# Optimization experiments

Measured on AMD Instinct MI355X. Metric: run time of the kernel, lower is better.

The kernel has to match this reference:

```python
import jax, jax.numpy as jnp
import numpy as np

B, D, L, H = 2, 64, 512, 1024  # batch, n_docs (timesteps), tokens per doc, bert hidden


def _ln(x, g, b):
    # torch.nn.LayerNorm over last dim, eps=1e-5
    m = jnp.mean(x, axis=-1, keepdims=True)
    v = jnp.mean((x - m) ** 2, axis=-1, keepdims=True)
    return (x - m) / jnp.sqrt(v + 1e-5) * g + b


def _ht(x):
    # Hardtanh(min=-8, max=8)
    return jnp.clip(x, -8.0, 8.0)


def setup_inputs() -> dict:
    key = jax.random.key(0)
    ks = jax.random.split(key, 12)
    xavier = lambda k, shape: jax.random.normal(k, shape, dtype=jnp.float32) * np.float32(np.sqrt(2.0 / sum(shape)))
    return {
        "trans": jax.random.normal(ks[0], (B, D, L, H), dtype=jnp.float32) * 0.1,  # frozen BERT last_hidden_state
        "document_mask": jax.random.bernoulli(ks[1], 0.9, (B, D)),
        "Wf": xavier(ks[2], (H, H)), "bf": jnp.ones((H,), jnp.float32),
        "Wi": xavier(ks[3], (H, H)), "bi": jnp.zeros((H,), jnp.float32),
        "Wg": xavier(ks[4], (H, H)), "bg": jnp.zeros((H,), jnp.float32),
        "Wo": xavier(ks[5], (H, H)), "bo": jnp.zeros((H,), jnp.float32),
        "Wp": xavier(ks[6], (H, H)), "bp": jnp.zeros((H,), jnp.float32),
        "tF": xavier(ks[7], (L,)), "tI": xavier(ks[8], (L,)), "tO": xavier(ks[9], (L,)),
        "c_gamma": jnp.ones((H,), jnp.float32), "c_beta": jnp.zeros((H,), jnp.float32),
        "h_gamma": jnp.ones((H,), jnp.float32), "h_beta": jnp.zeros((H,), jnp.float32),
    }


def _forward(trans, document_mask, Wf, bf, Wi, bi, Wg, bg, Wo, bo, Wp, bp,
             tF, tI, tO, c_gamma, c_beta, h_gamma, h_beta):
    b, d, l, h = trans.shape
    # docFlat @ transform: contract the token (l) axis -> [b, d, h]
    pF = jnp.einsum('bdlh,l->bdh', trans, tF)
    pI = jnp.einsum('bdlh,l->bdh', trans, tI)
    pO = jnp.einsum('bdlh,l->bdh', trans, tO)

    def step(carry, xs):
        c, hs = carry                      # each [b, h]
        pf, pi, po, m = xs                 # [b, h] x3, [b] bool
        nC = _ln(c, c_gamma, c_beta)
        nH = _ln(hs, h_gamma, h_beta)
        f = jax.nn.sigmoid(_ht(nH @ Wf.T + bf) + pf)
        c2 = c * f
        i = jax.nn.sigmoid(_ht(nH @ Wi.T + bi) + pi)
        g = _ht(jax.nn.gelu(nH @ Wg.T + bg, approximate=False) + pi)
        c2 = c2 + i * g
        o = jax.nn.sigmoid(_ht(nH @ Wo.T + bo) + po)
        h2 = o * _ht(jax.nn.gelu(nC @ Wp.T + bp, approximate=False))
        mm = m[:, None]
        h2 = jnp.where(mm, h2, hs)
        c2 = jnp.where(mm, c2, c)
        c2 = jnp.clip(c2, -10.0, 10.0)
        h2 = jnp.clip(h2, -10.0, 10.0)
        return (c2, h2), None

    init = (jnp.zeros((b, h), trans.dtype), jnp.zeros((b, h), trans.dtype))
    xs = (pF.transpose(1, 0, 2), pI.transpose(1, 0, 2), pO.transpose(1, 0, 2), document_mask.T)
    (c_fin, h_fin), _ = jax.lax.scan(step, init, xs)
    return h_fin  # [b, h] (original returns [b, h, 1])


def reference(trans, document_mask, Wf, bf, Wi, bi, Wg, bg, Wo, bo, Wp, bp,
              tF, tI, tO, c_gamma, c_beta, h_gamma, h_beta):
    return _forward(trans, document_mask, Wf, bf, Wi, bi, Wg, bg, Wo, bo, Wp, bp,
                    tF, tI, tO, c_gamma, c_beta, h_gamma, h_beta)
```

## Files before the change

### kernel.cpp

```cpp
#include <hip/hip_runtime.h>
#include <math.h>


#define NBLK 256

__device__ __forceinline__ float sigf(float x)   { return 1.0f / (1.0f + __expf(-x)); }
__device__ __forceinline__ float geluf(float x)  { return 0.5f * x * (1.0f + erff(x * 0.70710678118654752f)); }
__device__ __forceinline__ float clampf(float x, float lo, float hi) { return fminf(fmaxf(x, lo), hi); }

__device__ __forceinline__ void astf(float* p, float v) {
    __hip_atomic_store(p, v, __ATOMIC_RELAXED, __HIP_MEMORY_SCOPE_AGENT);
}
__device__ __forceinline__ float aldf(const float* p) {
    return __hip_atomic_load(p, __ATOMIC_RELAXED, __HIP_MEMORY_SCOPE_AGENT);
}
__device__ __forceinline__ void astu(unsigned* p, unsigned v) {
    __hip_atomic_store(p, v, __ATOMIC_RELAXED, __HIP_MEMORY_SCOPE_AGENT);
}
__device__ __forceinline__ unsigned aldu(const unsigned* p) {
    return __hip_atomic_load(p, __ATOMIC_RELAXED, __HIP_MEMORY_SCOPE_AGENT);
}

__device__ __forceinline__ void gridbar(unsigned tgt, unsigned* flags, unsigned* rel,
                                        int blk, int t) {
    __syncthreads();
    if (t == 0) astu(&flags[blk], tgt);
    if (blk == 0) {
        if (t < 64) {
            for (;;) {
                unsigned a = aldu(&flags[t]);
                unsigned b = aldu(&flags[t + 64]);
                unsigned c = aldu(&flags[t + 128]);
                unsigned d = aldu(&flags[t + 192]);
                int ok = (a >= tgt) && (b >= tgt) && (c >= tgt) && (d >= tgt);
                if (__all(ok)) break;
                __builtin_amdgcn_s_sleep(1);
            }
            if (t == 0) astu(rel, tgt);
        }
    } else if (t == 0) {
        while (aldu(rel) < tgt) __builtin_amdgcn_s_sleep(2);
    }
    __syncthreads();
}

__global__ __launch_bounds__(256, 1) void fused_kernel(
    const float* __restrict__ trans, const int* __restrict__ mask,
    const float* __restrict__ Wf, const float* __restrict__ bf,
    const float* __restrict__ Wi, const float* __restrict__ bi,
    const float* __restrict__ Wg, const float* __restrict__ bg,
    const float* __restrict__ Wo, const float* __restrict__ bo,
    const float* __restrict__ Wp, const float* __restrict__ bp,
    const float* __restrict__ tF, const float* __restrict__ tI, const float* __restrict__ tO,
    const float* __restrict__ c_gamma, const float* __restrict__ c_beta,
    const float* __restrict__ h_gamma, const float* __restrict__ h_beta,
    float* __restrict__ ws, float* __restrict__ out)
{
    const int t    = threadIdx.x;
    const int lane = t & 63;
    const int wv   = t >> 6;
    const int blk  = blockIdx.x;
    const int hrow = (blk << 2) + wv;

    unsigned* flags = (unsigned*)ws;
    unsigned* rel   = flags + 256;
    float* stC = ws + 320;
    float* stH = ws + 4416;
    float* pF  = ws + 8512;
    float* pI  = pF + 131072;
    float* pO  = pI + 131072;

    __shared__ float smem[4][1024];
    __shared__ float red[4][8];

    float4 wfr[4], wir[4], wgr[4], wor[4], wpr[4];
    {
        const float4* rf = (const float4*)(Wf + (size_t)hrow * 1024);
        const float4* ri = (const float4*)(Wi + (size_t)hrow * 1024);
        const float4* rg = (const float4*)(Wg + (size_t)hrow * 1024);
        const float4* ro = (const float4*)(Wo + (size_t)hrow * 1024);
        const float4* rp = (const float4*)(Wp + (size_t)hrow * 1024);
        #pragma unroll
        for (int q = 0; q < 4; ++q) {
            const int k4 = lane + 64 * q;
            wfr[q] = rf[k4]; wir[q] = ri[k4]; wgr[q] = rg[k4];
            wor[q] = ro[k4]; wpr[q] = rp[k4];
        }
    }
    const float bfv = bf[hrow], biv = bi[hrow], bgv = bg[hrow], bov = bo[hrow], bpv = bp[hrow];

    {
        float* sF = &smem[0][0];
        float* sI = &smem[0][512];
        float* sO = &smem[1][0];
        sF[t] = tF[t]; sF[t + 256] = tF[t + 256];
        sI[t] = tI[t]; sI[t + 256] = tI[t + 256];
        sO[t] = tO[t]; sO[t + 256] = tO[t + 256];
        __syncthreads();

        const int bd = blk >> 1;
        const int h0 = (blk & 1) * 512;
        const int s  = t & 127;
        const int g  = t >> 7;
        const float4* tr = (const float4*)trans + (size_t)bd * 512 * 256 + (h0 >> 2) + s;

        float4 aF = make_float4(0.f,0.f,0.f,0.f);
        float4 aI = make_float4(0.f,0.f,0.f,0.f);
        float4 aO = make_float4(0.f,0.f,0.f,0.f);
        #pragma unroll 8
        for (int li = 0; li < 256; ++li) {
            const int l = g + 2 * li;
            float4 v = tr[(size_t)l * 256];
            const float wf = sF[l], wi = sI[l], wo = sO[l];
            aF.x = fmaf(v.x, wf, aF.x); aF.y = fmaf(v.y, wf, aF.y);
            aF.z = fmaf(v.z, wf, aF.z); aF.w = fmaf(v.w, wf, aF.w);
            aI.x = fmaf(v.x, wi, aI.x); aI.y = fmaf(v.y, wi, aI.y);
            aI.z = fmaf(v.z, wi, aI.z); aI.w = fmaf(v.w, wi, aI.w);
            aO.x = fmaf(v.x, wo, aO.x); aO.y = fmaf(v.y, wo, aO.y);
            aO.z = fmaf(v.z, wo, aO.z); aO.w = fmaf(v.w, wo, aO.w);
        }
        float4* cmb = (float4*)&smem[2][0];
        if (g == 1) { cmb[s] = aF; cmb[128 + s] = aI; cmb[256 + s] = aO; }
        __syncthreads();
        if (g == 0) {
            const float4 bF = cmb[s], bI = cmb[128 + s], bO = cmb[256 + s];
            aF.x += bF.x; aF.y += bF.y; aF.z += bF.z; aF.w += bF.w;
            aI.x += bI.x; aI.y += bI.y; aI.z += bI.z; aI.w += bI.w;
            aO.x += bO.x; aO.y += bO.y; aO.z += bO.z; aO.w += bO.w;
            const int base = bd * 1024 + h0 + 4 * s;
            astf(&pF[base+0], aF.x); astf(&pF[base+1], aF.y);
            astf(&pF[base+2], aF.z); astf(&pF[base+3], aF.w);
            astf(&pI[base+0], aI.x); astf(&pI[base+1], aI.y);
            astf(&pI[base+2], aI.z); astf(&pI[base+3], aI.w);
            astf(&pO[base+0], aO.x); astf(&pO[base+1], aO.y);
            astf(&pO[base+2], aO.z); astf(&pO[base+3], aO.w);
        }
    }
    gridbar(1u, flags, rel, blk, t);

    float cgv[4], cbv[4], hgv[4], hbv[4];
    #pragma unroll
    for (int j = 0; j < 4; ++j) {
        const int e = t + 256 * j;
        cgv[j] = c_gamma[e]; cbv[j] = c_beta[e];
        hgv[j] = h_gamma[e]; hbv[j] = h_beta[e];
    }

    for (int d = 0; d < 64; ++d) {
        const int par = d & 1;
        const float* cc = stC + par * 2048;
        const float* hc = stH + par * 2048;
        float* cn = stC + (par ^ 1) * 2048;
        float* hn = stH + (par ^ 1) * 2048;

        float pfv = 0.f, piv = 0.f, pov = 0.f;
        if (lane < 2) {
            const int pidx = (lane * 64 + d) * 1024 + hrow;
            pfv = aldf(&pF[pidx]); piv = aldf(&pI[pidx]); pov = aldf(&pO[pidx]);
        }

        float cv0[4], cv1[4], hv0[4], hv1[4];
        float s0=0,s1=0,s2=0,s3=0,s4=0,s5=0,s6=0,s7=0;
        #pragma unroll
        for (int j = 0; j < 4; ++j) {
            const int e = t + 256 * j;
            cv0[j] = aldf(cc + e);        cv1[j] = aldf(cc + 1024 + e);
            hv0[j] = aldf(hc + e);        hv1[j] = aldf(hc + 1024 + e);
        }
        #pragma unroll
        for (int j = 0; j < 4; ++j) {
            s0 += cv0[j]; s1 += cv0[j]*cv0[j];
            s2 += cv1[j]; s3 += cv1[j]*cv1[j];
            s4 += hv0[j]; s5 += hv0[j]*hv0[j];
            s6 += hv1[j]; s7 += hv1[j]*hv1[j];
        }
        #pragma unroll
        for (int off = 32; off; off >>= 1) {
            s0 += __shfl_xor(s0, off); s1 += __shfl_xor(s1, off);
            s2 += __shfl_xor(s2, off); s3 += __shfl_xor(s3, off);
            s4 += __shfl_xor(s4, off); s5 += __shfl_xor(s5, off);
            s6 += __shfl_xor(s6, off); s7 += __shfl_xor(s7, off);
        }
        if (lane == 0) {
            red[wv][0]=s0; red[wv][1]=s1; red[wv][2]=s2; red[wv][3]=s3;
            red[wv][4]=s4; red[wv][5]=s5; red[wv][6]=s6; red[wv][7]=s7;
        }
        __syncthreads();
        const float tc0 = red[0][0]+red[1][0]+red[2][0]+red[3][0];
        const float qc0 = red[0][1]+red[1][1]+red[2][1]+red[3][1];
        const float tc1 = red[0][2]+red[1][2]+red[2][2]+red[3][2];
        const float qc1 = red[0][3]+red[1][3]+red[2][3]+red[3][3];
        const float th0 = red[0][4]+red[1][4]+red[2][4]+red[3][4];
        const float qh0 = red[0][5]+red[1][5]+red[2][5]+red[3][5];
        const float th1 = red[0][6]+red[1][6]+red[2][6]+red[3][6];
        const float qh1 = red[0][7]+red[1][7]+red[2][7]+red[3][7];
        const float inv = 1.0f / 1024.0f;
        const float mc0 = tc0*inv, rc0 = rsqrtf(qc0*inv - mc0*mc0 + 1e-5f);
        const float mc1 = tc1*inv, rc1 = rsqrtf(qc1*inv - mc1*mc1 + 1e-5f);
        const float mh0 = th0*inv, rh0 = rsqrtf(qh0*inv - mh0*mh0 + 1e-5f);
        const float mh1 = th1*inv, rh1 = rsqrtf(qh1*inv - mh1*mh1 + 1e-5f);

        #pragma unroll
        for (int j = 0; j < 4; ++j) {
            const int e = t + 256 * j;
            smem[0][e] = (hv0[j]-mh0)*rh0*hgv[j] + hbv[j];
            smem[1][e] = (hv1[j]-mh1)*rh1*hgv[j] + hbv[j];
            smem[2][e] = (cv0[j]-mc0)*rc0*cgv[j] + cbv[j];
            smem[3][e] = (cv1[j]-mc1)*rc1*cgv[j] + cbv[j];
        }
        __syncthreads();

        float zf0=0,zf1=0,zi0=0,zi1=0,zg0=0,zg1=0,zo0=0,zo1=0,zp0=0,zp1=0;
        #pragma unroll
        for (int q = 0; q < 4; ++q) {
            const int k4 = lane + 64 * q;
            const float4 n0 = ((const float4*)smem[0])[k4];
            const float4 n1 = ((const float4*)smem[1])[k4];
            const float4 m0 = ((const float4*)smem[2])[k4];
            const float4 m1 = ((const float4*)smem[3])[k4];
            zf0 += wfr[q].x*n0.x + wfr[q].y*n0.y + wfr[q].z*n0.z + wfr[q].w*n0.w;
            zf1 += wfr[q].x*n1.x + wfr[q].y*n1.y + wfr[q].z*n1.z + wfr[q].w*n1.w;
            zi0 += wir[q].x*n0.x + wir[q].y*n0.y + wir[q].z*n0.z + wir[q].w*n0.w;
            zi1 += wir[q].x*n1.x + wir[q].y*n1.y + wir[q].z*n1.z + wir[q].w*n1.w;
            zg0 += wgr[q].x*n0.x + wgr[q].y*n0.y + wgr[q].z*n0.z + wgr[q].w*n0.w;
            zg1 += wgr[q].x*n1.x + wgr[q].y*n1.y + wgr[q].z*n1.z + wgr[q].w*n1.w;
            zo0 += wor[q].x*n0.x + wor[q].y*n0.y + wor[q].z*n0.z + wor[q].w*n0.w;
            zo1 += wor[q].x*n1.x + wor[q].y*n1.y + wor[q].z*n1.z + wor[q].w*n1.w;
            zp0 += wpr[q].x*m0.x + wpr[q].y*m0.y + wpr[q].z*m0.z + wpr[q].w*m0.w;
            zp1 += wpr[q].x*m1.x + wpr[q].y*m1.y + wpr[q].z*m1.z + wpr[q].w*m1.w;
        }
        #pragma unroll
        for (int off = 32; off; off >>= 1) {
            zf0 += __shfl_xor(zf0, off); zf1 += __shfl_xor(zf1, off);
            zi0 += __shfl_xor(zi0, off); zi1 += __shfl_xor(zi1, off);
            zg0 += __shfl_xor(zg0, off); zg1 += __shfl_xor(zg1, off);
            zo0 += __shfl_xor(zo0, off); zo1 += __shfl_xor(zo1, off);
            zp0 += __shfl_xor(zp0, off); zp1 += __shfl_xor(zp1, off);
        }

        if (lane < 2) {
            const int b = lane;
            const float zf = b ? zf1 : zf0;
            const float zi = b ? zi1 : zi0;
            const float zg = b ? zg1 : zg0;
            const float zo = b ? zo1 : zo0;
            const float zp = b ? zp1 : zp0;
            const float f  = sigf(clampf(zf + bfv, -8.f, 8.f) + pfv);
            const float ig = sigf(clampf(zi + biv, -8.f, 8.f) + piv);
            const float g  = clampf(geluf(zg + bgv) + piv, -8.f, 8.f);
            const float o  = sigf(clampf(zo + bov, -8.f, 8.f) + pov);
            const float hp = clampf(geluf(zp + bpv), -8.f, 8.f);
            const float co = aldf(cc + b * 1024 + hrow);
            const float ho = aldf(hc + b * 1024 + hrow);
            float c2 = co * f + ig * g;
            float h2 = o * hp;
            if (mask[b * 64 + d] == 0) { c2 = co; h2 = ho; }
            c2 = clampf(c2, -10.f, 10.f);
            h2 = clampf(h2, -10.f, 10.f);
            if (d == 63) {
                out[b * 1024 + hrow] = h2;
            } else {
                astf(cn + b * 1024 + hrow, c2);
                astf(hn + b * 1024 + hrow, h2);
            }
        }

        if (d == 63) break;
        gridbar((unsigned)(d + 2), flags, rel, blk, t);
    }
}

extern "C" void kernel_launch(void* const* d_in, const int* in_sizes, int n_in,
                              void* d_out, int out_size, void* d_ws, size_t ws_size,
                              hipStream_t stream)
{
    const float* trans = (const float*)d_in[0];
    const int*   mask  = (const int*)d_in[1];
    const float* Wf = (const float*)d_in[2];  const float* bf = (const float*)d_in[3];
    const float* Wi = (const float*)d_in[4];  const float* bi = (const float*)d_in[5];
    const float* Wg = (const float*)d_in[6];  const float* bg = (const float*)d_in[7];
    const float* Wo = (const float*)d_in[8];  const float* bo = (const float*)d_in[9];
    const float* Wp = (const float*)d_in[10]; const float* bp = (const float*)d_in[11];
    const float* tF = (const float*)d_in[12];
    const float* tI = (const float*)d_in[13];
    const float* tO = (const float*)d_in[14];
    const float* c_gamma = (const float*)d_in[15];
    const float* c_beta  = (const float*)d_in[16];
    const float* h_gamma = (const float*)d_in[17];
    const float* h_beta  = (const float*)d_in[18];

    float* ws  = (float*)d_ws;
    float* out = (float*)d_out;

    hipMemsetAsync(d_ws, 0, 8512u * sizeof(float), stream);

    void* args[] = { (void*)&trans, (void*)&mask,
                     (void*)&Wf, (void*)&bf, (void*)&Wi, (void*)&bi,
                     (void*)&Wg, (void*)&bg, (void*)&Wo, (void*)&bo,
                     (void*)&Wp, (void*)&bp,
                     (void*)&tF, (void*)&tI, (void*)&tO,
                     (void*)&c_gamma, (void*)&c_beta, (void*)&h_gamma, (void*)&h_beta,
                     (void*)&ws, (void*)&out };
    hipLaunchCooperativeKernel((void*)fused_kernel, dim3(256), dim3(256), args, 0, stream);
}
```

Before: 830.7 us.

## Replace per-step grid barrier with tagged 64-bit state values and polling

```diff
diff --git a/kernel.cpp b/kernel.cpp
--- a/kernel.cpp
+++ b/kernel.cpp
@@ -3,6 +3,7 @@
 
 
 #define NBLK 256
+typedef unsigned long long u64;
 
 __device__ __forceinline__ float sigf(float x)   { return 1.0f / (1.0f + __expf(-x)); }
 __device__ __forceinline__ float geluf(float x)  { return 0.5f * x * (1.0f + erff(x * 0.70710678118654752f)); }
@@ -18,6 +19,12 @@
     __hip_atomic_store(p, v, __ATOMIC_RELAXED, __HIP_MEMORY_SCOPE_AGENT);
 }
 __device__ __forceinline__ unsigned aldu(const unsigned* p) {
+    return __hip_atomic_load(p, __ATOMIC_RELAXED, __HIP_MEMORY_SCOPE_AGENT);
+}
+__device__ __forceinline__ void ast64(u64* p, u64 v) {
+    __hip_atomic_store(p, v, __ATOMIC_RELAXED, __HIP_MEMORY_SCOPE_AGENT);
+}
+__device__ __forceinline__ u64 ald64(const u64* p) {
     return __hip_atomic_load(p, __ATOMIC_RELAXED, __HIP_MEMORY_SCOPE_AGENT);
 }
 
@@ -64,14 +71,14 @@
 
     unsigned* flags = (unsigned*)ws;
     unsigned* rel   = flags + 256;
-    float* stC = ws + 320;
-    float* stH = ws + 4416;
-    float* pF  = ws + 8512;
+    u64* stC2 = (u64*)(ws + 320);
+    u64* stH2 = (u64*)(ws + 8512);
+    float* pF  = ws + 16704;
     float* pI  = pF + 131072;
     float* pO  = pI + 131072;
 
-    __shared__ float smem[4][1024];
-    __shared__ float red[4][8];
+    __shared__ float smem[2][4][1024];
+    __shared__ float red[2][4][8];
 
     float4 wfr[4], wir[4], wgr[4], wor[4], wpr[4];
     {
@@ -90,9 +97,9 @@
     const float bfv = bf[hrow], biv = bi[hrow], bgv = bg[hrow], bov = bo[hrow], bpv = bp[hrow];
 
     {
-        float* sF = &smem[0][0];
-        float* sI = &smem[0][512];
-        float* sO = &smem[1][0];
+        float* sF = &smem[0][0][0];
+        float* sI = &smem[0][0][512];
+        float* sO = &smem[0][1][0];
         sF[t] = tF[t]; sF[t + 256] = tF[t + 256];
         sI[t] = tI[t]; sI[t + 256] = tI[t + 256];
         sO[t] = tO[t]; sO[t + 256] = tO[t + 256];
@@ -119,7 +126,7 @@
             aO.x = fmaf(v.x, wo, aO.x); aO.y = fmaf(v.y, wo, aO.y);
             aO.z = fmaf(v.z, wo, aO.z); aO.w = fmaf(v.w, wo, aO.w);
         }
-        float4* cmb = (float4*)&smem[2][0];
+        float4* cmb = (float4*)&smem[0][2][0];
         if (g == 1) { cmb[s] = aF; cmb[128 + s] = aI; cmb[256 + s] = aO; }
         __syncthreads();
         if (g == 0) {
@@ -148,10 +155,12 @@
 
     for (int d = 0; d < 64; ++d) {
         const int par = d & 1;
-        const float* cc = stC + par * 2048;
-        const float* hc = stH + par * 2048;
-        float* cn = stC + (par ^ 1) * 2048;
-        float* hn = stH + (par ^ 1) * 2048;
+        const u64* cc2 = stC2 + par * 2048;
+        const u64* hc2 = stH2 + par * 2048;
+        u64* cn2 = stC2 + (par ^ 1) * 2048;
+        u64* hn2 = stH2 + (par ^ 1) * 2048;
+        float (*sm)[1024] = smem[par];
+        float (*rd)[8]    = red[par];
 
         float pfv = 0.f, piv = 0.f, pov = 0.f;
         if (lane < 2) {
@@ -159,16 +168,39 @@
             pfv = aldf(&pF[pidx]); piv = aldf(&pI[pidx]); pov = aldf(&pO[pidx]);
         }
 
+        u64 vc0[4], vc1[4], vh0[4], vh1[4];
+        u64 vco = 0, vho = 0;
+        const unsigned dtag = (unsigned)d;
+        for (;;) {
+            #pragma unroll
+            for (int j = 0; j < 4; ++j) {
+                const int e = t + 256 * j;
+                vc0[j] = ald64(cc2 + e);        vc1[j] = ald64(cc2 + 1024 + e);
+                vh0[j] = ald64(hc2 + e);        vh1[j] = ald64(hc2 + 1024 + e);
+            }
+            bool ok = true;
+            #pragma unroll
+            for (int j = 0; j < 4; ++j) {
+                ok = ok && ((unsigned)(vc0[j] >> 32) == dtag) && ((unsigned)(vc1[j] >> 32) == dtag)
+                        && ((unsigned)(vh0[j] >> 32) == dtag) && ((unsigned)(vh1[j] >> 32) == dtag);
+            }
+            if (lane < 2) {
+                vco = ald64(cc2 + lane * 1024 + hrow);
+                vho = ald64(hc2 + lane * 1024 + hrow);
+                ok = ok && ((unsigned)(vco >> 32) == dtag) && ((unsigned)(vho >> 32) == dtag);
+            }
+            if (ok) break;
+            __builtin_amdgcn_s_sleep(1);
+        }
+
         float cv0[4], cv1[4], hv0[4], hv1[4];
         float s0=0,s1=0,s2=0,s3=0,s4=0,s5=0,s6=0,s7=0;
         #pragma unroll
         for (int j = 0; j < 4; ++j) {
-            const int e = t + 256 * j;
-            cv0[j] = aldf(cc + e);        cv1[j] = aldf(cc + 1024 + e);
-            hv0[j] = aldf(hc + e);        hv1[j] = aldf(hc + 1024 + e);
-        }
-        #pragma unroll
-        for (int j = 0; j < 4; ++j) {
+            cv0[j] = __uint_as_float((unsigned)vc0[j]);
+            cv1[j] = __uint_as_float((unsigned)vc1[j]);
+            hv0[j] = __uint_as_float((unsigned)vh0[j]);
+            hv1[j] = __uint_as_float((unsigned)vh1[j]);
             s0 += cv0[j]; s1 += cv0[j]*cv0[j];
             s2 += cv1[j]; s3 += cv1[j]*cv1[j];
             s4 += hv0[j]; s5 += hv0[j]*hv0[j];
@@ -182,18 +214,18 @@
             s6 += __shfl_xor(s6, off); s7 += __shfl_xor(s7, off);
         }
         if (lane == 0) {
-            red[wv][0]=s0; red[wv][1]=s1; red[wv][2]=s2; red[wv][3]=s3;
-            red[wv][4]=s4; red[wv][5]=s5; red[wv][6]=s6; red[wv][7]=s7;
+            rd[wv][0]=s0; rd[wv][1]=s1; rd[wv][2]=s2; rd[wv][3]=s3;
+            rd[wv][4]=s4; rd[wv][5]=s5; rd[wv][6]=s6; rd[wv][7]=s7;
         }
         __syncthreads();
-        const float tc0 = red[0][0]+red[1][0]+red[2][0]+red[3][0];
-        const float qc0 = red[0][1]+red[1][1]+red[2][1]+red[3][1];
-        const float tc1 = red[0][2]+red[1][2]+red[2][2]+red[3][2];
-        const float qc1 = red[0][3]+red[1][3]+red[2][3]+red[3][3];
-        const float th0 = red[0][4]+red[1][4]+red[2][4]+red[3][4];
-        const float qh0 = red[0][5]+red[1][5]+red[2][5]+red[3][5];
-        const float th1 = red[0][6]+red[1][6]+red[2][6]+red[3][6];
-        const float qh1 = red[0][7]+red[1][7]+red[2][7]+red[3][7];
+        const float tc0 = rd[0][0]+rd[1][0]+rd[2][0]+rd[3][0];
+        const float qc0 = rd[0][1]+rd[1][1]+rd[2][1]+rd[3][1];
+        const float tc1 = rd[0][2]+rd[1][2]+rd[2][2]+rd[3][2];
+        const float qc1 = rd[0][3]+rd[1][3]+rd[2][3]+rd[3][3];
+        const float th0 = rd[0][4]+rd[1][4]+rd[2][4]+rd[3][4];
+        const float qh0 = rd[0][5]+rd[1][5]+rd[2][5]+rd[3][5];
+        const float th1 = rd[0][6]+rd[1][6]+rd[2][6]+rd[3][6];
+        const float qh1 = rd[0][7]+rd[1][7]+rd[2][7]+rd[3][7];
         const float inv = 1.0f / 1024.0f;
         const float mc0 = tc0*inv, rc0 = rsqrtf(qc0*inv - mc0*mc0 + 1e-5f);
         const float mc1 = tc1*inv, rc1 = rsqrtf(qc1*inv - mc1*mc1 + 1e-5f);
@@ -203,10 +235,10 @@
         #pragma unroll
         for (int j = 0; j < 4; ++j) {
             const int e = t + 256 * j;
-            smem[0][e] = (hv0[j]-mh0)*rh0*hgv[j] + hbv[j];
-            smem[1][e] = (hv1[j]-mh1)*rh1*hgv[j] + hbv[j];
-            smem[2][e] = (cv0[j]-mc0)*rc0*cgv[j] + cbv[j];
-            smem[3][e] = (cv1[j]-mc1)*rc1*cgv[j] + cbv[j];
+            sm[0][e] = (hv0[j]-mh0)*rh0*hgv[j] + hbv[j];
+            sm[1][e] = (hv1[j]-mh1)*rh1*hgv[j] + hbv[j];
+            sm[2][e] = (cv0[j]-mc0)*rc0*cgv[j] + cbv[j];
+            sm[3][e] = (cv1[j]-mc1)*rc1*cgv[j] + cbv[j];
         }
         __syncthreads();
 
@@ -214,10 +246,10 @@
         #pragma unroll
         for (int q = 0; q < 4; ++q) {
             const int k4 = lane + 64 * q;
-            const float4 n0 = ((const float4*)smem[0])[k4];
-            const float4 n1 = ((const float4*)smem[1])[k4];
-            const float4 m0 = ((const float4*)smem[2])[k4];
-            const float4 m1 = ((const float4*)smem[3])[k4];
+            const float4 n0 = ((const float4*)sm[0])[k4];
+            const float4 n1 = ((const float4*)sm[1])[k4];
+            const float4 m0 = ((const float4*)sm[2])[k4];
+            const float4 m1 = ((const float4*)sm[3])[k4];
             zf0 += wfr[q].x*n0.x + wfr[q].y*n0.y + wfr[q].z*n0.z + wfr[q].w*n0.w;
             zf1 += wfr[q].x*n1.x + wfr[q].y*n1.y + wfr[q].z*n1.z + wfr[q].w*n1.w;
             zi0 += wir[q].x*n0.x + wir[q].y*n0.y + wir[q].z*n0.z + wir[q].w*n0.w;
@@ -250,8 +282,8 @@
             const float g  = clampf(geluf(zg + bgv) + piv, -8.f, 8.f);
             const float o  = sigf(clampf(zo + bov, -8.f, 8.f) + pov);
             const float hp = clampf(geluf(zp + bpv), -8.f, 8.f);
-            const float co = aldf(cc + b * 1024 + hrow);
-            const float ho = aldf(hc + b * 1024 + hrow);
+            const float co = __uint_as_float((unsigned)vco);
+            const float ho = __uint_as_float((unsigned)vho);
             float c2 = co * f + ig * g;
             float h2 = o * hp;
             if (mask[b * 64 + d] == 0) { c2 = co; h2 = ho; }
@@ -260,13 +292,11 @@
             if (d == 63) {
                 out[b * 1024 + hrow] = h2;
             } else {
-                astf(cn + b * 1024 + hrow, c2);
-                astf(hn + b * 1024 + hrow, h2);
-            }
-        }
-
-        if (d == 63) break;
-        gridbar((unsigned)(d + 2), flags, rel, blk, t);
+                const u64 tg = ((u64)(unsigned)(d + 1)) << 32;
+                ast64(cn2 + b * 1024 + hrow, tg | (u64)__float_as_uint(c2));
+                ast64(hn2 + b * 1024 + hrow, tg | (u64)__float_as_uint(h2));
+            }
+        }
     }
 }
 
@@ -292,7 +322,7 @@
     float* ws  = (float*)d_ws;
     float* out = (float*)d_out;
 
-    hipMemsetAsync(d_ws, 0, 8512u * sizeof(float), stream);
+    hipMemsetAsync(d_ws, 0, 16704u * sizeof(float), stream);
 
     void* args[] = { (void*)&trans, (void*)&mask,
                      (void*)&Wf, (void*)&bf, (void*)&Wi, (void*)&bi,
```

After: 966.5 us. 16.3% more time.
